# Optimization experiments

Hardware: AMD Instinct MI355X
Metric: run time of the kernel (lower is better)

## Reference

```python
import jax, jax.numpy as jnp
import numpy as np

VOCAB = 32000; DIM = 512; NL = 6; B = 2; L = 1024
DI = 2 * DIM      # d_inner (expand=2)
DS = 16           # d_state
DC = 4            # d_conv
DR = DIM // 16    # dt_rank = ceil(512/16) = 32


def setup_inputs() -> dict:
    key = jax.random.key(0)
    ks = jax.random.split(key, 10)
    s = 0.02
    tokens = jax.random.randint(ks[0], (B, L), 0, VOCAB)
    pos_emb = jax.random.normal(ks[1], (1, L, DIM)) * s
    embed = jax.random.normal(ks[2], (VOCAB, DIM)) * s
    lm_w = jax.random.normal(ks[3], (VOCAB, DIM)) * s
    lm_b = jnp.zeros((VOCAB,), jnp.float32)
    in_proj_w = jax.random.normal(ks[4], (NL, 2 * DI, DIM)) * s
    conv_w = jax.random.normal(ks[5], (NL, DI, DC)) * s
    conv_b = jnp.zeros((NL, DI), jnp.float32)
    x_proj_w = jax.random.normal(ks[6], (NL, DR + 2 * DS, DI)) * s
    dt_proj_w = jax.random.normal(ks[7], (NL, DI, DR)) * s
    dt_proj_b = jnp.broadcast_to(jnp.log(jnp.expm1(jnp.float32(0.01))), (NL, DI)).astype(jnp.float32)
    A_log = jnp.log(jnp.broadcast_to(jnp.arange(1, DS + 1, dtype=jnp.float32), (NL, DI, DS)))
    Dp = jnp.ones((NL, DI), jnp.float32)
    out_w = jax.random.normal(ks[8], (NL, DIM, DI)) * s
    ln_g = jnp.ones((NL, DIM), jnp.float32)
    ln_b = jnp.zeros((NL, DIM), jnp.float32)
    return dict(tokens=tokens, pos_emb=pos_emb, embed=embed, lm_w=lm_w, lm_b=lm_b,
                in_proj_w=in_proj_w, conv_w=conv_w, conv_b=conv_b, x_proj_w=x_proj_w,
                dt_proj_w=dt_proj_w, dt_proj_b=dt_proj_b, A_log=A_log, Dp=Dp,
                out_w=out_w, ln_g=ln_g, ln_b=ln_b)


def silu(x):
    return x * jax.nn.sigmoid(x)


def layernorm(x, g, b, eps=1e-5):
    mu = jnp.mean(x, -1, keepdims=True)
    var = jnp.var(x, -1, keepdims=True)
    return (x - mu) * jax.lax.rsqrt(var + eps) * g + b


def causal_dwconv(x, w, b):
    # x: (B,L,DI), w: (DI,DC) depthwise, left-pad causal
    xp = jnp.pad(x, ((0, 0), (DC - 1, 0), (0, 0)))
    y = b
    for k in range(DC):
        y = y + w[:, k] * xp[:, k:k + x.shape[1], :]
    return y


def selective_scan(u, dt, A, Bm, Cm, Dp):
    # u,dt: (B,L,DI); A: (DI,DS); Bm,Cm: (B,L,DS)
    dA = jnp.exp(dt[..., None] * A)                       # (B,L,DI,DS)
    dBu = dt[..., None] * Bm[:, :, None, :] * u[..., None]
    h0 = jnp.zeros((u.shape[0], DI, DS), u.dtype)

    def step(h, inp):
        dA_t, dBu_t, C_t = inp
        h = dA_t * h + dBu_t
        y = jnp.einsum('bdn,bn->bd', h, C_t)
        return h, y

    _, ys = jax.lax.scan(step, h0, (dA.transpose(1, 0, 2, 3),
                                    dBu.transpose(1, 0, 2, 3),
                                    Cm.transpose(1, 0, 2)))
    return ys.transpose(1, 0, 2) + u * Dp


def mamba_block(x, in_w, cw, cb, xp_w, dtw, dtb, A_log, Dp, ow):
    xz = jnp.einsum('bld,ed->ble', x, in_w)               # (B,L,2*DI)
    xc, z = jnp.split(xz, 2, axis=-1)
    xc = silu(causal_dwconv(xc, cw, cb))
    x_dbl = jnp.einsum('bld,ed->ble', xc, xp_w)           # (B,L,DR+2*DS)
    dt, Bm, Cm = jnp.split(x_dbl, [DR, DR + DS], axis=-1)
    dt = jax.nn.softplus(jnp.einsum('blr,dr->bld', dt, dtw) + dtb)
    A = -jnp.exp(A_log)
    y = selective_scan(xc, dt, A, Bm, Cm, Dp)
    y = y * silu(z)
    return jnp.einsum('bld,ed->ble', y, ow)


def reference(tokens, pos_emb, embed, lm_w, lm_b, in_proj_w, conv_w, conv_b,
              x_proj_w, dt_proj_w, dt_proj_b, A_log, Dp, out_w, ln_g, ln_b):
    x = embed[tokens] + pos_emb[:, :tokens.shape[1]]
    for i in range(NL):
        res = x
        x = mamba_block(x, in_proj_w[i], conv_w[i], conv_b[i], x_proj_w[i],
                        dt_proj_w[i], dt_proj_b[i], A_log[i], Dp[i], out_w[i])
        x = layernorm(x + res, ln_g[i], ln_b[i])
    return jnp.einsum('bld,vd->blv', x, lm_w) + lm_b
```

## Files before the change

### kernel.cpp

```cpp
#include <hip/hip_runtime.h>
#include <hip/hip_bf16.h>
#include <math.h>

#define BB 2
#define LL 1024
#define DIM 512
#define NL 6
#define DI 1024
#define DS 16
#define DC 4
#define DR 32
#define VOCAB 32000
#define M_ROWS (BB * LL)
#define CCH 64
#define CHLEN (LL / CCH)
#define KSPLIT 8
#define OSPLIT 4

typedef unsigned short u16;
typedef __attribute__((ext_vector_type(8))) short bf16x8;
typedef __attribute__((ext_vector_type(4))) float f32x4;

__device__ __forceinline__ u16 f2bf(float f) {
    unsigned u = __float_as_uint(f);
    u += 0x7FFF + ((u >> 16) & 1);
    return (u16)(u >> 16);
}
__device__ __forceinline__ float bf2f(u16 h) {
    return __uint_as_float(((unsigned)h) << 16);
}
#define SWZ(r, c) ((c) ^ (((r) >> 1) & 3))

__global__ __launch_bounds__(256) void cast_all(const float* __restrict__ lm,
                                                const float* __restrict__ inw,
                                                const float* __restrict__ ow,
                                                const float* __restrict__ xp,
                                                u16* __restrict__ lmb,
                                                u16* __restrict__ inb,
                                                u16* __restrict__ owb_,
                                                u16* __restrict__ xpb) {
    int idx = blockIdx.x * 256 + threadIdx.x;
    const float* src; u16* dst; int off;
    if (idx < 2048000)      { src = lm;  dst = lmb;  off = idx; }
    else if (idx < 2834432) { src = inw; dst = inb;  off = idx - 2048000; }
    else if (idx < 3227648) { src = ow;  dst = owb_; off = idx - 2834432; }
    else                    { src = xp;  dst = xpb;  off = idx - 3227648; }
    float4 v0 = ((const float4*)src)[off * 2];
    float4 v1 = ((const float4*)src)[off * 2 + 1];
    union { u16 h[8]; int4 v; } r;
    r.h[0] = f2bf(v0.x); r.h[1] = f2bf(v0.y); r.h[2] = f2bf(v0.z); r.h[3] = f2bf(v0.w);
    r.h[4] = f2bf(v1.x); r.h[5] = f2bf(v1.y); r.h[6] = f2bf(v1.z); r.h[7] = f2bf(v1.w);
    ((int4*)dst)[off] = r.v;
}

__global__ __launch_bounds__(256) void embed_kernel(const int* __restrict__ tok,
                                                    const float* __restrict__ pos,
                                                    const float* __restrict__ emb,
                                                    float* __restrict__ x,
                                                    u16* __restrict__ xb) {
    int idx = blockIdx.x * 256 + threadIdx.x;
    int d = idx & (DIM - 1);
    int l = (idx >> 9) & (LL - 1);
    int b = idx >> 19;
    int t = tok[b * LL + l];
    float v = emb[(size_t)t * DIM + d] + pos[l * DIM + d];
    x[idx] = v;
    xb[idx] = f2bf(v);
}

__global__ __launch_bounds__(256) void gemm_n64(const u16* __restrict__ A,
                                                const u16* __restrict__ W,
                                                float* __restrict__ out,
                                                u16* __restrict__ outb,
                                                const float* __restrict__ bias,
                                                int lda, int ldw, int ldc,
                                                int KS, int pstride) {
    __shared__ __align__(16) char smem_raw[24576];
    u16* As = (u16*)smem_raw;
    u16* Ws = (u16*)(smem_raw + 16384);
    float* Cs = (float*)smem_raw;

    const int t = threadIdx.x;
    const int l = t & 63;
    const int w = t >> 6;
    const int gx = gridDim.x, gy = gridDim.y;
    const int nwg = gx * gy * gridDim.z;
    const int fid = (blockIdx.z * gy + blockIdx.y) * gx + blockIdx.x;
    const int q8 = nwg >> 3, r8 = nwg & 7;
    const int xcd = fid & 7, rank = fid >> 3;
    const int wgid = (xcd < r8 ? xcd * (q8 + 1) : r8 * (q8 + 1) + (xcd - r8) * q8) + rank;
    const int kz = wgid % gx;
    const int bm = ((wgid / gx) % gy) * 128;
    const int bnn = (wgid / (gx * gy)) * 64;
    const int wm = w * 32;

    f32x4 acc[2][4] = {};
    const int nt = KS >> 5;
    const int kbeg = kz * KS;

    auto STAGE = [&](int bufi, int k0) {
#pragma unroll
        for (int p = 0; p < 2; ++p) {
            const int i = p * 256 + w * 64 + l;
            const int row = i >> 2;
            const int kq = SWZ(row, i & 3);
            __builtin_amdgcn_global_load_lds(
                (const __attribute__((address_space(1))) unsigned int*)
                    (A + (size_t)(bm + row) * lda + k0 + kq * 8),
                (__attribute__((address_space(3))) unsigned int*)
                    (As + bufi * 4096 + (p * 256 + w * 64) * 8),
                16, 0, 0);
        }
        {
            const int i = w * 64 + l;
            const int row = i >> 2;
            const int kq = SWZ(row, i & 3);
            __builtin_amdgcn_global_load_lds(
                (const __attribute__((address_space(1))) unsigned int*)
                    (W + (size_t)(bnn + row) * ldw + k0 + kq * 8),
                (__attribute__((address_space(3))) unsigned int*)
                    (Ws + bufi * 2048 + (w * 64) * 8),
                16, 0, 0);
        }
    };
    auto COMPUTE = [&](int bufi) {
        const u16* Ab = As + bufi * 4096;
        const u16* Wb = Ws + bufi * 2048;
#pragma unroll
        for (int mi = 0; mi < 2; ++mi) {
            const int ar = wm + mi * 16 + (l & 15);
            bf16x8 a = *(const bf16x8*)(Ab + ar * 32 + SWZ(ar, l >> 4) * 8);
#pragma unroll
            for (int ni = 0; ni < 4; ++ni) {
                const int wr = ni * 16 + (l & 15);
                bf16x8 b = *(const bf16x8*)(Wb + wr * 32 + SWZ(wr, l >> 4) * 8);
                acc[mi][ni] = __builtin_amdgcn_mfma_f32_16x16x32_bf16(b, a, acc[mi][ni], 0, 0, 0);
            }
        }
    };

    STAGE(0, kbeg);
    for (int tt = 0; tt < nt; ++tt) {
        if (tt + 1 < nt) {
            STAGE((tt + 1) & 1, kbeg + ((tt + 1) << 5));
            asm volatile("s_waitcnt vmcnt(3)\ns_barrier" ::: "memory");
        } else {
            asm volatile("s_waitcnt vmcnt(0)\ns_barrier" ::: "memory");
        }
        COMPUTE(tt & 1);
        asm volatile("s_waitcnt lgkmcnt(0)\ns_barrier" ::: "memory");
    }

    if (outb != nullptr) {
        u16* opb = outb + (size_t)kz * pstride;
#pragma unroll
        for (int mi = 0; mi < 2; ++mi) {
            const int row = bm + wm + mi * 16 + (l & 15);
#pragma unroll
            for (int ni = 0; ni < 4; ++ni) {
                const int col = bnn + ni * 16 + ((l >> 4) << 2);
                ushort4 v;
                v.x = f2bf(acc[mi][ni][0]); v.y = f2bf(acc[mi][ni][1]);
                v.z = f2bf(acc[mi][ni][2]); v.w = f2bf(acc[mi][ni][3]);
                *(ushort4*)(opb + (size_t)row * ldc + col) = v;
            }
        }
    } else {
        float* op = out + (size_t)kz * pstride;
#pragma unroll
        for (int pass = 0; pass < 2; ++pass) {
            if ((w >> 1) == pass) {
                const int rbase = (w & 1) * 32;
#pragma unroll
                for (int mi = 0; mi < 2; ++mi) {
                    const int r = rbase + mi * 16 + (l & 15);
#pragma unroll
                    for (int ni = 0; ni < 4; ++ni) {
                        const int c = ni * 16 + ((l >> 4) << 2);
                        float4 v;
                        v.x = acc[mi][ni][0]; v.y = acc[mi][ni][1];
                        v.z = acc[mi][ni][2]; v.w = acc[mi][ni][3];
                        *(float4*)(Cs + r * 65 + c) = v;
                    }
                }
            }
            __syncthreads();
#pragma unroll
            for (int it = 0; it < 4; ++it) {
                const int idx = it * 256 + t;
                const int r = idx >> 4;
                const int c4 = (idx & 15) * 4;
                float4 v = *(float4*)(Cs + r * 65 + c4);
                if (bias != nullptr) {
                    float4 b4 = *(const float4*)(bias + bnn + c4);
                    v.x += b4.x; v.y += b4.y; v.z += b4.z; v.w += b4.w;
                }
                *(float4*)(op + (size_t)(bm + pass * 64 + r) * ldc + bnn + c4) = v;
            }
            __syncthreads();
        }
    }
}

__global__ __launch_bounds__(256) void xdred_dt(const float* __restrict__ Pf,
                                                const float* __restrict__ dtw,
                                                const float* __restrict__ dtb,
                                                float* __restrict__ xd,
                                                float* __restrict__ dt) {
    __shared__ float xds[64];
    const int m = blockIdx.x;
    const int t = threadIdx.x;
    if (t < 64) {
        float s = 0.f;
#pragma unroll
        for (int kz = 0; kz < KSPLIT; ++kz)
            s += Pf[(size_t)kz * (M_ROWS * 64) + m * 64 + t];
        xds[t] = s;
        xd[m * 64 + t] = s;
    }
    __syncthreads();
    const int d0 = t * 4;
    const float4 bv = *(const float4*)(dtb + d0);
    float a0 = bv.x, a1 = bv.y, a2 = bv.z, a3 = bv.w;
    const float* w0p = dtw + (size_t)(d0 + 0) * DR;
    const float* w1p = dtw + (size_t)(d0 + 1) * DR;
    const float* w2p = dtw + (size_t)(d0 + 2) * DR;
    const float* w3p = dtw + (size_t)(d0 + 3) * DR;
#pragma unroll
    for (int k = 0; k < DR; k += 4) {
        float4 xv = *(const float4*)&xds[k];
        float4 w0 = *(const float4*)(w0p + k);
        float4 w1 = *(const float4*)(w1p + k);
        float4 w2 = *(const float4*)(w2p + k);
        float4 w3 = *(const float4*)(w3p + k);
        a0 += w0.x * xv.x + w0.y * xv.y + w0.z * xv.z + w0.w * xv.w;
        a1 += w1.x * xv.x + w1.y * xv.y + w1.z * xv.z + w1.w * xv.w;
        a2 += w2.x * xv.x + w2.y * xv.y + w2.z * xv.z + w2.w * xv.w;
        a3 += w3.x * xv.x + w3.y * xv.y + w3.z * xv.z + w3.w * xv.w;
    }
    a0 = (a0 > 20.f) ? a0 : log1pf(__expf(a0));
    a1 = (a1 > 20.f) ? a1 : log1pf(__expf(a1));
    a2 = (a2 > 20.f) ? a2 : log1pf(__expf(a2));
    a3 = (a3 > 20.f) ? a3 : log1pf(__expf(a3));
    float4 v; v.x = a0; v.y = a1; v.z = a2; v.w = a3;
    *(float4*)(dt + (size_t)m * DI + d0) = v;
}

__global__ __launch_bounds__(256) void conv_silu(const u16* __restrict__ xzb,
                                                 const float* __restrict__ cw,
                                                 const float* __restrict__ cb,
                                                 u16* __restrict__ xcb) {
    int idx = blockIdx.x * 256 + threadIdx.x;
    int c = idx & (DI - 1);
    int l = (idx >> 10) & (LL - 1);
    int b = idx >> 20;
    float acc = cb[c];
#pragma unroll
    for (int k = 0; k < DC; ++k) {
        int ll = l + k - (DC - 1);
        if (ll >= 0)
            acc += cw[c * DC + k] * bf2f(xzb[((size_t)(b * LL + ll)) * (2 * DI) + c]);
    }
    float v = acc / (1.f + __expf(-acc));
    xcb[idx] = f2bf(v);
}

__global__ __launch_bounds__(256) void scan_pass1(const u16* __restrict__ xcb,
                                                  const float* __restrict__ dt,
                                                  const float* __restrict__ xdbl,
                                                  const float* __restrict__ A_log,
                                                  float* __restrict__ S,
                                                  float* __restrict__ Q) {
    const int d = blockIdx.x * 256 + threadIdx.x;
    const int b = blockIdx.y;
    const int c = blockIdx.z;
    float a[DS];
#pragma unroll
    for (int q = 0; q < 4; ++q) {
        float4 al = *(const float4*)(A_log + d * DS + q * 4);
        a[q * 4 + 0] = -__expf(al.x);
        a[q * 4 + 1] = -__expf(al.y);
        a[q * 4 + 2] = -__expf(al.z);
        a[q * 4 + 3] = -__expf(al.w);
    }
    float Qr[DS];
#pragma unroll
    for (int n = 0; n < DS; ++n) Qr[n] = 0.f;
    float Ssum = 0.f;

    const int l0 = c * CHLEN;
    const float* dtp = dt + ((size_t)b * LL + l0) * DI + d;
    const u16*   up  = xcb + ((size_t)b * LL + l0) * DI + d;
    const float* xdp = xdbl + ((size_t)b * LL + l0) * 64 + DR;

    for (int l = 0; l < CHLEN; ++l) {
        float dtv = dtp[(size_t)l * DI];
        float uv  = bf2f(up[(size_t)l * DI]);
        float wv = dtv * uv;
        Ssum += dtv;
#pragma unroll
        for (int q = 0; q < 4; ++q) {
            float4 Bv = *(const float4*)(xdp + l * 64 + q * 4);
            float dA0 = __expf(dtv * a[q * 4 + 0]);
            float dA1 = __expf(dtv * a[q * 4 + 1]);
            float dA2 = __expf(dtv * a[q * 4 + 2]);
            float dA3 = __expf(dtv * a[q * 4 + 3]);
            Qr[q * 4 + 0] = dA0 * Qr[q * 4 + 0] + wv * Bv.x;
            Qr[q * 4 + 1] = dA1 * Qr[q * 4 + 1] + wv * Bv.y;
            Qr[q * 4 + 2] = dA2 * Qr[q * 4 + 2] + wv * Bv.z;
            Qr[q * 4 + 3] = dA3 * Qr[q * 4 + 3] + wv * Bv.w;
        }
    }
    S[((size_t)b * CCH + c) * DI + d] = Ssum;
    float* Qp = Q + (((size_t)b * CCH + c) * DI + d) * DS;
#pragma unroll
    for (int q = 0; q < 4; ++q) {
        float4 o;
        o.x = Qr[q * 4 + 0]; o.y = Qr[q * 4 + 1];
        o.z = Qr[q * 4 + 2]; o.w = Qr[q * 4 + 3];
        *(float4*)(Qp + q * 4) = o;
    }
}

__global__ __launch_bounds__(64) void scan_pass2(const float* __restrict__ A_log,
                                                 const float* __restrict__ S,
                                                 float* __restrict__ Q) {
    const int idx = blockIdx.x * 64 + threadIdx.x;
    const int b = idx >> 14;
    const int dn = idx & 16383;
    const int d = dn >> 4;
    const float a = -__expf(A_log[dn]);
    float h = 0.f;
    for (int c = 0; c < CCH; ++c) {
        const size_t soff = ((size_t)b * CCH + c) * DI + d;
        const size_t qoff = ((size_t)b * CCH + c) * (size_t)(DI * DS) + dn;
        float P = __expf(a * S[soff]);
        float qv = Q[qoff];
        Q[qoff] = h;
        h = P * h + qv;
    }
}

__global__ __launch_bounds__(256) void scan_pass3(const u16* __restrict__ xcb,
                                                  const float* __restrict__ dt,
                                                  const float* __restrict__ xdbl,
                                                  const u16* __restrict__ xzb,
                                                  const float* __restrict__ A_log,
                                                  const float* __restrict__ Dpp,
                                                  const float* __restrict__ Q,
                                                  u16* __restrict__ y) {
    const int d = blockIdx.x * 256 + threadIdx.x;
    const int b = blockIdx.y;
    const int c = blockIdx.z;
    float a[DS];
#pragma unroll
    for (int q = 0; q < 4; ++q) {
        float4 al = *(const float4*)(A_log + d * DS + q * 4);
        a[q * 4 + 0] = -__expf(al.x);
        a[q * 4 + 1] = -__expf(al.y);
        a[q * 4 + 2] = -__expf(al.z);
        a[q * 4 + 3] = -__expf(al.w);
    }
    float h[DS];
    const float* Qp = Q + (((size_t)b * CCH + c) * DI + d) * DS;
#pragma unroll
    for (int q = 0; q < 4; ++q) {
        float4 hv = *(const float4*)(Qp + q * 4);
        h[q * 4 + 0] = hv.x; h[q * 4 + 1] = hv.y;
        h[q * 4 + 2] = hv.z; h[q * 4 + 3] = hv.w;
    }
    const float dp = Dpp[d];

    const int l0 = c * CHLEN;
    const float* dtp = dt + ((size_t)b * LL + l0) * DI + d;
    const u16*   up  = xcb + ((size_t)b * LL + l0) * DI + d;
    const float* xdp = xdbl + ((size_t)b * LL + l0) * 64 + DR;
    const u16* zp = xzb + ((size_t)b * LL + l0) * (2 * DI) + DI + d;
    u16* yp = y + ((size_t)b * LL + l0) * DI + d;

    for (int l = 0; l < CHLEN; ++l) {
        float dtv = dtp[(size_t)l * DI];
        float uv  = bf2f(up[(size_t)l * DI]);
        float wv = dtv * uv;
        float p = 0.f;
#pragma unroll
        for (int q = 0; q < 4; ++q) {
            float4 Bv = *(const float4*)(xdp + l * 64 + q * 4);
            float4 Cv = *(const float4*)(xdp + l * 64 + 16 + q * 4);
            float dA0 = __expf(dtv * a[q * 4 + 0]);
            float dA1 = __expf(dtv * a[q * 4 + 1]);
            float dA2 = __expf(dtv * a[q * 4 + 2]);
            float dA3 = __expf(dtv * a[q * 4 + 3]);
            h[q * 4 + 0] = dA0 * h[q * 4 + 0] + wv * Bv.x;
            h[q * 4 + 1] = dA1 * h[q * 4 + 1] + wv * Bv.y;
            h[q * 4 + 2] = dA2 * h[q * 4 + 2] + wv * Bv.z;
            h[q * 4 + 3] = dA3 * h[q * 4 + 3] + wv * Bv.w;
            p += h[q * 4 + 0] * Cv.x + h[q * 4 + 1] * Cv.y +
                 h[q * 4 + 2] * Cv.z + h[q * 4 + 3] * Cv.w;
        }
        float zv = bf2f(zp[(size_t)l * (2 * DI)]);
        float g = zv / (1.f + __expf(-zv));
        yp[(size_t)l * DI] = f2bf((p + uv * dp) * g);
    }
}

__global__ __launch_bounds__(256) void add_ln(const float* __restrict__ opart,
                                              float* __restrict__ x,
                                              const float* __restrict__ g,
                                              const float* __restrict__ b,
                                              u16* __restrict__ xb) {
    const int PS = M_ROWS * DIM;
    int m = blockIdx.x;
    int t = threadIdx.x;
    const float* xr = x + (size_t)m * DIM;
    float v0 = xr[t];
    float v1 = xr[t + 256];
#pragma unroll
    for (int kz = 0; kz < OSPLIT; ++kz) {
        const float* op = opart + (size_t)kz * PS + (size_t)m * DIM;
        v0 += op[t];
        v1 += op[t + 256];
    }
    float s = v0 + v1;
    float ss = v0 * v0 + v1 * v1;
#pragma unroll
    for (int off = 32; off > 0; off >>= 1) {
        s += __shfl_down(s, off, 64);
        ss += __shfl_down(ss, off, 64);
    }
    __shared__ float sb[4], ssb[4];
    int w = t >> 6;
    if ((t & 63) == 0) { sb[w] = s; ssb[w] = ss; }
    __syncthreads();
    float stot = sb[0] + sb[1] + sb[2] + sb[3];
    float sstot = ssb[0] + ssb[1] + ssb[2] + ssb[3];
    float mean = stot * (1.f / DIM);
    float var = sstot * (1.f / DIM) - mean * mean;
    float rs = rsqrtf(var + 1e-5f);
    float* xw = x + (size_t)m * DIM;
    float o0 = (v0 - mean) * rs * g[t] + b[t];
    float o1 = (v1 - mean) * rs * g[t + 256] + b[t + 256];
    xw[t] = o0;
    xw[t + 256] = o1;
    xb[(size_t)m * DIM + t] = f2bf(o0);
    xb[(size_t)m * DIM + t + 256] = f2bf(o1);
}

extern "C" void kernel_launch(void* const* d_in, const int* in_sizes, int n_in,
                              void* d_out, int out_size, void* d_ws, size_t ws_size,
                              hipStream_t stream) {
    const int*   tokens = (const int*)d_in[0];
    const float* pos    = (const float*)d_in[1];
    const float* emb    = (const float*)d_in[2];
    const float* lm_w   = (const float*)d_in[3];
    const float* lm_b   = (const float*)d_in[4];
    const float* in_w   = (const float*)d_in[5];
    const float* cw     = (const float*)d_in[6];
    const float* cb     = (const float*)d_in[7];
    const float* xpw    = (const float*)d_in[8];
    const float* dtw    = (const float*)d_in[9];
    const float* dtb    = (const float*)d_in[10];
    const float* A_log  = (const float*)d_in[11];
    const float* Dpp    = (const float*)d_in[12];
    const float* ow     = (const float*)d_in[13];
    const float* lng    = (const float*)d_in[14];
    const float* lnb    = (const float*)d_in[15];
    float* out = (float*)d_out;

    float* ws = (float*)d_ws;
    float* x    = ws;
    float* xd   = x + 1048576;
    float* dt   = xd + 131072;
    float* S    = dt + 2097152;
    float* Qb   = S + 131072;
    float* Pf   = Qb + 2097152;
    float* Pf2  = Pf + 1048576;
    u16* xzb    = (u16*)(Pf2 + 4194304);
    u16* xb     = xzb + 4194304;
    u16* yb     = xb + 1048576;
    u16* xcb    = yb + 2097152;
    u16* lm_wb  = xcb + 2097152;
    u16* in_wb  = lm_wb + 16384000;
    u16* owb    = in_wb + 6291456;
    u16* xpwb   = owb + 3145728;

    cast_all<<<12800, 256, 0, stream>>>(lm_w, in_w, ow, xpw,
                                        lm_wb, in_wb, owb, xpwb);

    embed_kernel<<<M_ROWS * DIM / 256, 256, 0, stream>>>(tokens, pos, emb, x, xb);

    for (int i = 0; i < NL; ++i) {
        gemm_n64<<<dim3(1, M_ROWS / 128, 2048 / 64), 256, 0, stream>>>(
            xb, in_wb + (size_t)i * 2048 * 512, nullptr, xzb, nullptr,
            512, 512, 2048, 512, 0);
        conv_silu<<<M_ROWS * DI / 256, 256, 0, stream>>>(
            xzb, cw + (size_t)i * DI * DC, cb + (size_t)i * DI, xcb);
        gemm_n64<<<dim3(KSPLIT, M_ROWS / 128, 1), 256, 0, stream>>>(
            xcb, xpwb + (size_t)i * 64 * 1024, Pf, nullptr, nullptr,
            1024, 1024, 64, 1024 / KSPLIT, M_ROWS * 64);
        xdred_dt<<<M_ROWS, 256, 0, stream>>>(
            Pf, dtw + (size_t)i * DI * DR, dtb + (size_t)i * DI, xd, dt);
        scan_pass1<<<dim3(DI / 256, BB, CCH), 256, 0, stream>>>(
            xcb, dt, xd, A_log + (size_t)i * DI * DS, S, Qb);
        scan_pass2<<<(BB * DI * DS) / 64, 64, 0, stream>>>(
            A_log + (size_t)i * DI * DS, S, Qb);
        scan_pass3<<<dim3(DI / 256, BB, CCH), 256, 0, stream>>>(
            xcb, dt, xd, xzb, A_log + (size_t)i * DI * DS, Dpp + (size_t)i * DI, Qb, yb);
        gemm_n64<<<dim3(OSPLIT, M_ROWS / 128, 512 / 64), 256, 0, stream>>>(
            yb, owb + (size_t)i * 512 * 1024, Pf2, nullptr, nullptr,
            1024, 1024, 512, 1024 / OSPLIT, M_ROWS * 512);
        add_ln<<<M_ROWS, 256, 0, stream>>>(
            Pf2, x, lng + (size_t)i * DIM, lnb + (size_t)i * DIM, xb);
    }

    gemm_n64<<<dim3(1, M_ROWS / 128, VOCAB / 64), 256, 0, stream>>>(
        xb, lm_wb, out, nullptr, lm_b,
        512, 512, VOCAB, 512, 0);
}
```

Baseline: 851.1 us.

## Fuse split-K reduction and dt projection into scan passes, vectorize conv

Removes the separate xdred_dt kernel: scan_pass1 and scan_pass3 each reduce the split-K x_proj partials for their chunk into shared memory and recompute the dt projection plus softplus per element, so the full fp32 dt tensor is never written to or read from global memory. conv_silu now handles 8 channels per thread with vector loads and stores. The GEMM inner loop preloads the four B fragments once per k-step before the MFMAs. The cost is that the dt matvec and split-K reduction are computed twice (once per scan pass), along with extra shared memory and register pressure in the scan kernels.

```diff
diff --git a/kernel.cpp b/kernel.cpp
--- a/kernel.cpp
+++ b/kernel.cpp
@@ -126,16 +126,19 @@
     auto COMPUTE = [&](int bufi) {
         const u16* Ab = As + bufi * 4096;
         const u16* Wb = Ws + bufi * 2048;
+        bf16x8 bfr[4];
+#pragma unroll
+        for (int ni = 0; ni < 4; ++ni) {
+            const int wr = ni * 16 + (l & 15);
+            bfr[ni] = *(const bf16x8*)(Wb + wr * 32 + SWZ(wr, l >> 4) * 8);
+        }
 #pragma unroll
         for (int mi = 0; mi < 2; ++mi) {
             const int ar = wm + mi * 16 + (l & 15);
             bf16x8 a = *(const bf16x8*)(Ab + ar * 32 + SWZ(ar, l >> 4) * 8);
 #pragma unroll
-            for (int ni = 0; ni < 4; ++ni) {
-                const int wr = ni * 16 + (l & 15);
-                bf16x8 b = *(const bf16x8*)(Wb + wr * 32 + SWZ(wr, l >> 4) * 8);
-                acc[mi][ni] = __builtin_amdgcn_mfma_f32_16x16x32_bf16(b, a, acc[mi][ni], 0, 0, 0);
-            }
+            for (int ni = 0; ni < 4; ++ni)
+                acc[mi][ni] = __builtin_amdgcn_mfma_f32_16x16x32_bf16(bfr[ni], a, acc[mi][ni], 0, 0, 0);
         }
     };
 
@@ -202,78 +205,77 @@
     }
 }
 
-__global__ __launch_bounds__(256) void xdred_dt(const float* __restrict__ Pf,
-                                                const float* __restrict__ dtw,
-                                                const float* __restrict__ dtb,
-                                                float* __restrict__ xd,
-                                                float* __restrict__ dt) {
-    __shared__ float xds[64];
-    const int m = blockIdx.x;
-    const int t = threadIdx.x;
-    if (t < 64) {
-        float s = 0.f;
-#pragma unroll
-        for (int kz = 0; kz < KSPLIT; ++kz)
-            s += Pf[(size_t)kz * (M_ROWS * 64) + m * 64 + t];
-        xds[t] = s;
-        xd[m * 64 + t] = s;
-    }
-    __syncthreads();
-    const int d0 = t * 4;
-    const float4 bv = *(const float4*)(dtb + d0);
-    float a0 = bv.x, a1 = bv.y, a2 = bv.z, a3 = bv.w;
-    const float* w0p = dtw + (size_t)(d0 + 0) * DR;
-    const float* w1p = dtw + (size_t)(d0 + 1) * DR;
-    const float* w2p = dtw + (size_t)(d0 + 2) * DR;
-    const float* w3p = dtw + (size_t)(d0 + 3) * DR;
-#pragma unroll
-    for (int k = 0; k < DR; k += 4) {
-        float4 xv = *(const float4*)&xds[k];
-        float4 w0 = *(const float4*)(w0p + k);
-        float4 w1 = *(const float4*)(w1p + k);
-        float4 w2 = *(const float4*)(w2p + k);
-        float4 w3 = *(const float4*)(w3p + k);
-        a0 += w0.x * xv.x + w0.y * xv.y + w0.z * xv.z + w0.w * xv.w;
-        a1 += w1.x * xv.x + w1.y * xv.y + w1.z * xv.z + w1.w * xv.w;
-        a2 += w2.x * xv.x + w2.y * xv.y + w2.z * xv.z + w2.w * xv.w;
-        a3 += w3.x * xv.x + w3.y * xv.y + w3.z * xv.z + w3.w * xv.w;
-    }
-    a0 = (a0 > 20.f) ? a0 : log1pf(__expf(a0));
-    a1 = (a1 > 20.f) ? a1 : log1pf(__expf(a1));
-    a2 = (a2 > 20.f) ? a2 : log1pf(__expf(a2));
-    a3 = (a3 > 20.f) ? a3 : log1pf(__expf(a3));
-    float4 v; v.x = a0; v.y = a1; v.z = a2; v.w = a3;
-    *(float4*)(dt + (size_t)m * DI + d0) = v;
-}
-
 __global__ __launch_bounds__(256) void conv_silu(const u16* __restrict__ xzb,
                                                  const float* __restrict__ cw,
                                                  const float* __restrict__ cb,
                                                  u16* __restrict__ xcb) {
-    int idx = blockIdx.x * 256 + threadIdx.x;
-    int c = idx & (DI - 1);
-    int l = (idx >> 10) & (LL - 1);
-    int b = idx >> 20;
-    float acc = cb[c];
+    int idx8 = blockIdx.x * 256 + threadIdx.x;
+    int c0 = (idx8 & 127) * 8;
+    int m = idx8 >> 7;
+    int l = m & (LL - 1);
+
+    float acc[8];
+    float4 cb0 = *(const float4*)(cb + c0);
+    float4 cb1 = *(const float4*)(cb + c0 + 4);
+    acc[0] = cb0.x; acc[1] = cb0.y; acc[2] = cb0.z; acc[3] = cb0.w;
+    acc[4] = cb1.x; acc[5] = cb1.y; acc[6] = cb1.z; acc[7] = cb1.w;
 #pragma unroll
     for (int k = 0; k < DC; ++k) {
         int ll = l + k - (DC - 1);
-        if (ll >= 0)
-            acc += cw[c * DC + k] * bf2f(xzb[((size_t)(b * LL + ll)) * (2 * DI) + c]);
-    }
-    float v = acc / (1.f + __expf(-acc));
-    xcb[idx] = f2bf(v);
+        if (ll < 0) continue;
+        const u16* row = xzb + ((size_t)(m + k - (DC - 1))) * (2 * DI) + c0;
+        ushort4 r0 = *(const ushort4*)row;
+        ushort4 r1 = *(const ushort4*)(row + 4);
+#pragma unroll
+        for (int j = 0; j < 4; ++j) {
+            acc[j]     += cw[(c0 + j) * DC + k]     * bf2f(((const u16*)&r0)[j]);
+            acc[j + 4] += cw[(c0 + j + 4) * DC + k] * bf2f(((const u16*)&r1)[j]);
+        }
+    }
+    ushort4 o0, o1;
+#pragma unroll
+    for (int j = 0; j < 4; ++j) {
+        float v0 = acc[j]     / (1.f + __expf(-acc[j]));
+        float v1 = acc[j + 4] / (1.f + __expf(-acc[j + 4]));
+        ((u16*)&o0)[j] = f2bf(v0);
+        ((u16*)&o1)[j] = f2bf(v1);
+    }
+    u16* op = xcb + (size_t)idx8 * 8;
+    *(ushort4*)op = o0;
+    *(ushort4*)(op + 4) = o1;
 }
 
 __global__ __launch_bounds__(256) void scan_pass1(const u16* __restrict__ xcb,
-                                                  const float* __restrict__ dt,
-                                                  const float* __restrict__ xdbl,
+                                                  const float* __restrict__ Pf,
+                                                  const float* __restrict__ dtw,
+                                                  const float* __restrict__ dtb,
                                                   const float* __restrict__ A_log,
                                                   float* __restrict__ S,
                                                   float* __restrict__ Q) {
-    const int d = blockIdx.x * 256 + threadIdx.x;
+    __shared__ float xds[CHLEN][64];
+    const int t = threadIdx.x;
+    const int d = blockIdx.x * 256 + t;
     const int b = blockIdx.y;
     const int c = blockIdx.z;
+    const int l0 = c * CHLEN;
+    const int m0 = b * LL + l0;
+
+    for (int i = t; i < CHLEN * 64; i += 256) {
+        int r = i >> 6, cc = i & 63;
+        float s = 0.f;
+#pragma unroll
+        for (int kz = 0; kz < KSPLIT; ++kz)
+            s += Pf[(size_t)kz * (M_ROWS * 64) + (m0 + r) * 64 + cc];
+        xds[r][cc] = s;
+    }
+    __syncthreads();
+
+    float4 wreg[8];
+#pragma unroll
+    for (int kk = 0; kk < 8; ++kk)
+        wreg[kk] = *(const float4*)(dtw + (size_t)d * DR + kk * 4);
+    const float dtbv = dtb[d];
+
     float a[DS];
 #pragma unroll
     for (int q = 0; q < 4; ++q) {
@@ -288,19 +290,23 @@
     for (int n = 0; n < DS; ++n) Qr[n] = 0.f;
     float Ssum = 0.f;
 
-    const int l0 = c * CHLEN;
-    const float* dtp = dt + ((size_t)b * LL + l0) * DI + d;
-    const u16*   up  = xcb + ((size_t)b * LL + l0) * DI + d;
-    const float* xdp = xdbl + ((size_t)b * LL + l0) * 64 + DR;
+    const u16* up = xcb + (size_t)m0 * DI + d;
 
     for (int l = 0; l < CHLEN; ++l) {
-        float dtv = dtp[(size_t)l * DI];
-        float uv  = bf2f(up[(size_t)l * DI]);
+        float dacc = dtbv;
+#pragma unroll
+        for (int kk = 0; kk < 8; ++kk) {
+            float4 xv = *(const float4*)&xds[l][kk * 4];
+            dacc += wreg[kk].x * xv.x + wreg[kk].y * xv.y +
+                    wreg[kk].z * xv.z + wreg[kk].w * xv.w;
+        }
+        float dtv = (dacc > 20.f) ? dacc : log1pf(__expf(dacc));
+        float uv = bf2f(up[(size_t)l * DI]);
         float wv = dtv * uv;
         Ssum += dtv;
 #pragma unroll
         for (int q = 0; q < 4; ++q) {
-            float4 Bv = *(const float4*)(xdp + l * 64 + q * 4);
+            float4 Bv = *(const float4*)&xds[l][32 + q * 4];
             float dA0 = __expf(dtv * a[q * 4 + 0]);
             float dA1 = __expf(dtv * a[q * 4 + 1]);
             float dA2 = __expf(dtv * a[q * 4 + 2]);
@@ -342,16 +348,38 @@
 }
 
 __global__ __launch_bounds__(256) void scan_pass3(const u16* __restrict__ xcb,
-                                                  const float* __restrict__ dt,
-                                                  const float* __restrict__ xdbl,
+                                                  const float* __restrict__ Pf,
+                                                  const float* __restrict__ dtw,
+                                                  const float* __restrict__ dtb,
                                                   const u16* __restrict__ xzb,
                                                   const float* __restrict__ A_log,
                                                   const float* __restrict__ Dpp,
                                                   const float* __restrict__ Q,
                                                   u16* __restrict__ y) {
-    const int d = blockIdx.x * 256 + threadIdx.x;
+    __shared__ float xds[CHLEN][64];
+    const int t = threadIdx.x;
+    const int d = blockIdx.x * 256 + t;
     const int b = blockIdx.y;
     const int c = blockIdx.z;
+    const int l0 = c * CHLEN;
+    const int m0 = b * LL + l0;
+
+    for (int i = t; i < CHLEN * 64; i += 256) {
+        int r = i >> 6, cc = i & 63;
+        float s = 0.f;
+#pragma unroll
+        for (int kz = 0; kz < KSPLIT; ++kz)
+            s += Pf[(size_t)kz * (M_ROWS * 64) + (m0 + r) * 64 + cc];
+        xds[r][cc] = s;
+    }
+    __syncthreads();
+
+    float4 wreg[8];
+#pragma unroll
+    for (int kk = 0; kk < 8; ++kk)
+        wreg[kk] = *(const float4*)(dtw + (size_t)d * DR + kk * 4);
+    const float dtbv = dtb[d];
+
     float a[DS];
 #pragma unroll
     for (int q = 0; q < 4; ++q) {
@@ -371,22 +399,26 @@
     }
     const float dp = Dpp[d];
 
-    const int l0 = c * CHLEN;
-    const float* dtp = dt + ((size_t)b * LL + l0) * DI + d;
-    const u16*   up  = xcb + ((size_t)b * LL + l0) * DI + d;
-    const float* xdp = xdbl + ((size_t)b * LL + l0) * 64 + DR;
-    const u16* zp = xzb + ((size_t)b * LL + l0) * (2 * DI) + DI + d;
-    u16* yp = y + ((size_t)b * LL + l0) * DI + d;
+    const u16* up = xcb + (size_t)m0 * DI + d;
+    const u16* zp = xzb + (size_t)m0 * (2 * DI) + DI + d;
+    u16* yp = y + (size_t)m0 * DI + d;
 
     for (int l = 0; l < CHLEN; ++l) {
-        float dtv = dtp[(size_t)l * DI];
-        float uv  = bf2f(up[(size_t)l * DI]);
+        float dacc = dtbv;
+#pragma unroll
+        for (int kk = 0; kk < 8; ++kk) {
+            float4 xv = *(const float4*)&xds[l][kk * 4];
+            dacc += wreg[kk].x * xv.x + wreg[kk].y * xv.y +
+                    wreg[kk].z * xv.z + wreg[kk].w * xv.w;
+        }
+        float dtv = (dacc > 20.f) ? dacc : log1pf(__expf(dacc));
+        float uv = bf2f(up[(size_t)l * DI]);
         float wv = dtv * uv;
         float p = 0.f;
 #pragma unroll
         for (int q = 0; q < 4; ++q) {
-            float4 Bv = *(const float4*)(xdp + l * 64 + q * 4);
-            float4 Cv = *(const float4*)(xdp + l * 64 + 16 + q * 4);
+            float4 Bv = *(const float4*)&xds[l][32 + q * 4];
+            float4 Cv = *(const float4*)&xds[l][48 + q * 4];
             float dA0 = __expf(dtv * a[q * 4 + 0]);
             float dA1 = __expf(dtv * a[q * 4 + 1]);
             float dA2 = __expf(dtv * a[q * 4 + 2]);
@@ -469,9 +501,7 @@
 
     float* ws = (float*)d_ws;
     float* x    = ws;
-    float* xd   = x + 1048576;
-    float* dt   = xd + 131072;
-    float* S    = dt + 2097152;
+    float* S    = x + 1048576;
     float* Qb   = S + 131072;
     float* Pf   = Qb + 2097152;
     float* Pf2  = Pf + 1048576;
@@ -493,19 +523,19 @@
         gemm_n64<<<dim3(1, M_ROWS / 128, 2048 / 64), 256, 0, stream>>>(
             xb, in_wb + (size_t)i * 2048 * 512, nullptr, xzb, nullptr,
             512, 512, 2048, 512, 0);
-        conv_silu<<<M_ROWS * DI / 256, 256, 0, stream>>>(
+        conv_silu<<<M_ROWS * DI / 8 / 256, 256, 0, stream>>>(
             xzb, cw + (size_t)i * DI * DC, cb + (size_t)i * DI, xcb);
         gemm_n64<<<dim3(KSPLIT, M_ROWS / 128, 1), 256, 0, stream>>>(
             xcb, xpwb + (size_t)i * 64 * 1024, Pf, nullptr, nullptr,
             1024, 1024, 64, 1024 / KSPLIT, M_ROWS * 64);
-        xdred_dt<<<M_ROWS, 256, 0, stream>>>(
-            Pf, dtw + (size_t)i * DI * DR, dtb + (size_t)i * DI, xd, dt);
         scan_pass1<<<dim3(DI / 256, BB, CCH), 256, 0, stream>>>(
-            xcb, dt, xd, A_log + (size_t)i * DI * DS, S, Qb);
+            xcb, Pf, dtw + (size_t)i * DI * DR, dtb + (size_t)i * DI,
+            A_log + (size_t)i * DI * DS, S, Qb);
         scan_pass2<<<(BB * DI * DS) / 64, 64, 0, stream>>>(
             A_log + (size_t)i * DI * DS, S, Qb);
         scan_pass3<<<dim3(DI / 256, BB, CCH), 256, 0, stream>>>(
-            xcb, dt, xd, xzb, A_log + (size_t)i * DI * DS, Dpp + (size_t)i * DI, Qb, yb);
+            xcb, Pf, dtw + (size_t)i * DI * DR, dtb + (size_t)i * DI, xzb,
+            A_log + (size_t)i * DI * DS, Dpp + (size_t)i * DI, Qb, yb);
         gemm_n64<<<dim3(OSPLIT, M_ROWS / 128, 512 / 64), 256, 0, stream>>>(
             yb, owb + (size_t)i * 512 * 1024, Pf2, nullptr, nullptr,
             1024, 1024, 512, 1024 / OSPLIT, M_ROWS * 512);
```

After: 851.0 us. About the same (-0.0%).
